# Performance work log

Measured on AMD Instinct MI355X. Metric: run time of the kernel, lower is better.

## Reference

```python
import jax, jax.numpy as jnp
import numpy as np

B, S, D, H = 2, 2048, 768, 12
DK = D // H


def setup_inputs() -> dict:
    key = jax.random.key(0)
    ks = jax.random.split(key, 11)
    sc = 1.0 / np.sqrt(D)
    return {
        "q": jax.random.normal(ks[0], (B, S, D), jnp.float32),
        "k": jax.random.normal(ks[1], (B, S, D), jnp.float32),
        "v": jax.random.normal(ks[2], (B, S, D), jnp.float32),
        "Wq": jax.random.normal(ks[3], (D, D), jnp.float32) * sc,
        "bq": jnp.zeros((D,), jnp.float32),
        "Wk": jax.random.normal(ks[4], (D, D), jnp.float32) * sc,
        "bk": jnp.zeros((D,), jnp.float32),
        "Wv": jax.random.normal(ks[5], (D, D), jnp.float32) * sc,
        "bv": jnp.zeros((D,), jnp.float32),
        "Wc": jax.random.normal(ks[6], (D, D), jnp.float32) * sc,
        "bc": jnp.zeros((D,), jnp.float32),
    }


def _split(t):
    # Faithful to source: view(B, n_head, S, d_k) WITHOUT transpose —
    # heads partition the flattened (S*D) buffer, not the feature axis.
    return t.reshape(B, H, S, DK)


def reference(q, k, v, Wq, bq, Wk, bk, Wv, bv, Wc, bc):
    q = _split(q @ Wq.T + bq)  # [B,H,S,DK]
    k = _split(k @ Wk.T + bk)
    v = _split(v @ Wv.T + bv)
    score = jnp.einsum("bhqd,bhkd->bhqk", q, k) / np.sqrt(DK)  # [B,H,S,S]
    attn = jax.nn.softmax(score, axis=-1)
    # Faithful bug in source: uses pre-softmax score, not attn.
    out = jnp.einsum("bhqk,bhkd->bhqd", score, v)  # [B,H,S,DK]
    out = out.transpose(0, 2, 1, 3).reshape(B, S, D)  # concat
    out = out @ Wc.T + bc
    return out, attn
```

## Files before the change

kernel.cpp:

```cpp
#include <hip/hip_runtime.h>
#include <hip/hip_bf16.h>


#define S_LEN   2048
#define D_MODEL 768
#define NHEAD   12
#define DKH     64
#define BSROWS  4096
#define HEADSZ  (S_LEN * DKH)
#define WELEMS  (D_MODEL * D_MODEL)

typedef __attribute__((ext_vector_type(4))) float f32x4;
typedef __attribute__((ext_vector_type(8))) short s16x8;

static __device__ __forceinline__ unsigned cvtpk(float lo, float hi) {
    unsigned r;
    asm("v_cvt_pk_bf16_f32 %0, %1, %2" : "=v"(r) : "v"(lo), "v"(hi));
    return r;
}

static __device__ __forceinline__ short f2bf(float f) {
    return (short)cvtpk(f, f);
}

static __device__ __forceinline__ s16x8 cvt8(f32x4 a, f32x4 b) {
    union { unsigned u[4]; s16x8 v; } o;
    o.u[0] = cvtpk(a[0], a[1]);
    o.u[1] = cvtpk(a[2], a[3]);
    o.u[2] = cvtpk(b[0], b[1]);
    o.u[3] = cvtpk(b[2], b[3]);
    return o.v;
}

static __device__ __forceinline__ void gload16(const void* g, void* l) {
    __builtin_amdgcn_global_load_lds((const __attribute__((address_space(1))) void*)g,
                                     (__attribute__((address_space(3))) void*)l, 16, 0, 0);
}

static __device__ __forceinline__ s16x8 ldfrag(const short* tile, int row, int c16) {
    int byte = row * 128 + ((c16 * 16) ^ ((row & 7) << 4));
    return *(const s16x8*)((const char*)tile + byte);
}

__global__ __launch_bounds__(256) void prep_w(const float* __restrict__ W0,
                                              const float* __restrict__ W1,
                                              const float* __restrict__ W2,
                                              const float* __restrict__ W3,
                                              short* __restrict__ dst)
{
    const float* src = (blockIdx.y == 0) ? W0 : (blockIdx.y == 1) ? W1
                     : (blockIdx.y == 2) ? W2 : W3;
    short* d = dst + (size_t)blockIdx.y * WELEMS;
    int i = (blockIdx.x * 256 + threadIdx.x) * 8;
    f32x4 a = *(const f32x4*)(src + i);
    f32x4 b = *(const f32x4*)(src + i + 4);
    *(s16x8*)(d + i) = cvt8(a, b);
}

template<int A_F32, int OUT_F32>
static __device__ __forceinline__ void gemm_body128(const void* __restrict__ Av,
                                                    const short* __restrict__ Wb,
                                                    const float* __restrict__ bias,
                                                    void* __restrict__ Cv,
                                                    int mt, int nt)
{
    __shared__ short As[8192];
    __shared__ short Bs[8192];
    const int t = threadIdx.x, w = t >> 6, lane = t & 63;
    const int lrow = lane & 15, lgrp = lane >> 4;
    const int wr = w >> 1, wc = w & 1;

    f32x4 acc[4][4];
#pragma unroll
    for (int m = 0; m < 4; ++m)
#pragma unroll
        for (int n = 0; n < 4; ++n) acc[m][n] = {0.f, 0.f, 0.f, 0.f};

    for (int kk = 0; kk < 768; kk += 64) {
        __syncthreads();
#pragma unroll
        for (int j = 0; j < 4; ++j) {
            int cid = t + j * 256, row = cid >> 3, ch = cid & 7;
            gload16(Wb + (size_t)(nt * 128 + row) * 768 + kk + ((ch ^ (row & 7)) * 8),
                    (char*)Bs + j * 4096 + w * 1024);
        }
        if (A_F32) {
#pragma unroll
            for (int j = 0; j < 2; ++j) {
                int cid = t + j * 256, row = cid >> 2, q4 = cid & 3;
                const float* src = (const float*)Av + (size_t)(mt * 128 + row) * 768 + kk + q4 * 16;
                f32x4 v0 = *(const f32x4*)(src);
                f32x4 v1 = *(const f32x4*)(src + 4);
                f32x4 v2 = *(const f32x4*)(src + 8);
                f32x4 v3 = *(const f32x4*)(src + 12);
                int c0 = q4 * 2;
                *(s16x8*)((char*)As + row * 128 + (((c0    ) ^ (row & 7)) * 16)) = cvt8(v0, v1);
                *(s16x8*)((char*)As + row * 128 + (((c0 + 1) ^ (row & 7)) * 16)) = cvt8(v2, v3);
            }
        } else {
#pragma unroll
            for (int j = 0; j < 4; ++j) {
                int cid = t + j * 256, row = cid >> 3, ch = cid & 7;
                gload16((const short*)Av + (size_t)(mt * 128 + row) * 768 + kk + ((ch ^ (row & 7)) * 8),
                        (char*)As + j * 4096 + w * 1024);
            }
        }
        __syncthreads();
#pragma unroll
        for (int kc = 0; kc < 2; ++kc) {
            s16x8 af[4], bfr[4];
#pragma unroll
            for (int m = 0; m < 4; ++m) af[m] = ldfrag(As, wr * 64 + m * 16 + lrow, kc * 4 + lgrp);
#pragma unroll
            for (int n = 0; n < 4; ++n) bfr[n] = ldfrag(Bs, wc * 64 + n * 16 + lrow, kc * 4 + lgrp);
            __builtin_amdgcn_s_setprio(1);
#pragma unroll
            for (int m = 0; m < 4; ++m)
#pragma unroll
                for (int n = 0; n < 4; ++n)
                    acc[m][n] = __builtin_amdgcn_mfma_f32_16x16x32_bf16(af[m], bfr[n], acc[m][n], 0, 0, 0);
            __builtin_amdgcn_s_setprio(0);
        }
    }
#pragma unroll
    for (int n = 0; n < 4; ++n) {
        int col = nt * 128 + wc * 64 + n * 16 + lrow;
        float bvv = bias[col];
#pragma unroll
        for (int m = 0; m < 4; ++m)
#pragma unroll
            for (int r = 0; r < 4; ++r) {
                int row = mt * 128 + wr * 64 + m * 16 + lgrp * 4 + r;
                float v = acc[m][n][r] + bvv;
                if (OUT_F32) ((float*)Cv)[(size_t)row * 768 + col] = v;
                else         ((short*)Cv)[(size_t)row * 768 + col] = f2bf(v);
            }
    }
}

template<int OUT_F32>
static __device__ __forceinline__ void gemm_body64(const short* __restrict__ Av,
                                                   const short* __restrict__ Wb,
                                                   const float* __restrict__ bias,
                                                   void* __restrict__ Cv,
                                                   int mt, int nt)
{
    __shared__ short As[4096];
    __shared__ short Bs[4096];
    const int t = threadIdx.x, w = t >> 6, lane = t & 63;
    const int lrow = lane & 15, lgrp = lane >> 4;
    const int wr = w >> 1, wc = w & 1;

    f32x4 acc[2][2];
#pragma unroll
    for (int m = 0; m < 2; ++m)
#pragma unroll
        for (int n = 0; n < 2; ++n) acc[m][n] = {0.f, 0.f, 0.f, 0.f};

    for (int kk = 0; kk < 768; kk += 64) {
        __syncthreads();
#pragma unroll
        for (int j = 0; j < 2; ++j) {
            int cid = t + j * 256, row = cid >> 3, ch = cid & 7;
            int cs = (ch ^ (row & 7)) * 8;
            gload16(Av + (size_t)(mt * 64 + row) * 768 + kk + cs,
                    As + w * 512 + j * 2048);
            gload16(Wb + (size_t)(nt * 64 + row) * 768 + kk + cs,
                    Bs + w * 512 + j * 2048);
        }
        __syncthreads();
#pragma unroll
        for (int kc = 0; kc < 2; ++kc) {
            s16x8 af[2], bfr[2];
#pragma unroll
            for (int m = 0; m < 2; ++m) af[m] = ldfrag(As, wr * 32 + m * 16 + lrow, kc * 4 + lgrp);
#pragma unroll
            for (int n = 0; n < 2; ++n) bfr[n] = ldfrag(Bs, wc * 32 + n * 16 + lrow, kc * 4 + lgrp);
            __builtin_amdgcn_s_setprio(1);
#pragma unroll
            for (int m = 0; m < 2; ++m)
#pragma unroll
                for (int n = 0; n < 2; ++n)
                    acc[m][n] = __builtin_amdgcn_mfma_f32_16x16x32_bf16(af[m], bfr[n], acc[m][n], 0, 0, 0);
            __builtin_amdgcn_s_setprio(0);
        }
    }
#pragma unroll
    for (int n = 0; n < 2; ++n) {
        int col = nt * 64 + wc * 32 + n * 16 + lrow;
        float bvv = bias[col];
#pragma unroll
        for (int m = 0; m < 2; ++m)
#pragma unroll
            for (int r = 0; r < 4; ++r) {
                int row = mt * 64 + wr * 32 + m * 16 + lgrp * 4 + r;
                float v = acc[m][n][r] + bvv;
                if (OUT_F32) ((float*)Cv)[(size_t)row * 768 + col] = v;
                else         ((short*)Cv)[(size_t)row * 768 + col] = f2bf(v);
            }
    }
}

__global__ __launch_bounds__(256) void gemm_qkv(const float* __restrict__ q,
                                                const float* __restrict__ k,
                                                const float* __restrict__ v,
                                                const short* __restrict__ Wbf,
                                                const float* __restrict__ bq,
                                                const float* __restrict__ bk,
                                                const float* __restrict__ bv,
                                                short* __restrict__ Qw,
                                                short* __restrict__ Kw,
                                                short* __restrict__ Vw)
{
    const int bid = blockIdx.x;
    const int idx = bid >> 3;
    const int panel = (bid & 7) * 12 + idx / 6;
    const int nt = idx % 6;
    const int z = panel / 32, mt = panel % 32;
    const float* A; const float* bias; short* C;
    if (z == 0)      { A = q; bias = bq; C = Qw; }
    else if (z == 1) { A = k; bias = bk; C = Kw; }
    else             { A = v; bias = bv; C = Vw; }
    gemm_body128<1, 0>(A, Wbf + (size_t)z * WELEMS, bias, C, mt, nt);
}

__global__ __launch_bounds__(256) void gemm_out(const short* __restrict__ Ob,
                                                const short* __restrict__ Wcb,
                                                const float* __restrict__ bc,
                                                float* __restrict__ out)
{
    const int bid = blockIdx.x;
    const int idx = (bid & 7) * 96 + (bid >> 3);
    const int mt = idx / 12, nt = idx % 12;
    gemm_body64<1>(Ob, Wcb, bc, out, mt, nt);
}

__global__ __launch_bounds__(256) void vtrans(const short* __restrict__ Vw,
                                              short* __restrict__ Vt)
{
    const int sblk = blockIdx.x, bh = blockIdx.y;
    const short* src = Vw + (size_t)bh * HEADSZ;
    short* dst = Vt + (size_t)bh * HEADSZ;
    const int t = threadIdx.x;
#pragma unroll
    for (int j = 0; j < 2; ++j) {
        int cid = t + j * 256, dk = cid >> 3, ch = cid & 7;
        int s0 = sblk * 64 + ch * 8;
        s16x8 vv;
#pragma unroll
        for (int e = 0; e < 8; ++e) vv[e] = src[(size_t)(s0 + e) * DKH + dk];
        *(s16x8*)(dst + (size_t)dk * S_LEN + s0) = vv;
    }
}

__global__ __launch_bounds__(256, 4) void attn_fused2(const short* __restrict__ Qb,
                                                      const short* __restrict__ Kb,
                                                      const short* __restrict__ Vtb,
                                                      short* __restrict__ Ob,
                                                      float* __restrict__ attn)
{
    __shared__ short lds[20480];
    short* Qs = lds;
    const float CE = 0.18033688f;

    const int bid = blockIdx.x;
    const int swz = (bid & 7) * 96 + (bid >> 3);
    const int qb = swz & 31, bh = swz >> 5;
    const int t = threadIdx.x, w = t >> 6, lane = t & 63;
    const int lrow = lane & 15, lgrp = lane >> 4;
    const int qh = w & 1, kh = w >> 1;
    const int b = bh / NHEAD, h = bh % NHEAD;
    const short* Qh = Qb + (size_t)bh * HEADSZ;
    const short* Kh = Kb + (size_t)bh * HEADSZ;
    const short* Vth = Vtb + (size_t)bh * HEADSZ;
    const int q0 = qb * 64;

#define STAGE_K4(dst, kt) do {                                                  \
    _Pragma("unroll")                                                           \
    for (int j = 0; j < 2; ++j) {                                               \
        int cid = t + j * 256, row = cid >> 3, ch = cid & 7;                    \
        gload16(Kh + (size_t)((kt) * 64 + row) * DKH + ((ch ^ (row & 7)) * 8),  \
                (dst) + w * 512 + j * 2048);                                    \
    } } while (0)

#define STAGE_V4(dst, kt) do {                                                  \
    _Pragma("unroll")                                                           \
    for (int j = 0; j < 2; ++j) {                                               \
        int cid = t + j * 256, row = cid >> 3, ch = cid & 7;                    \
        gload16(Vth + (size_t)row * S_LEN + (kt) * 64 + ((ch ^ (row & 7)) * 8), \
                (dst) + w * 512 + j * 2048);                                    \
    } } while (0)

#pragma unroll
    for (int j = 0; j < 2; ++j) {
        int cid = t + j * 256, row = cid >> 3, ch = cid & 7;
        gload16(Qh + (size_t)(q0 + row) * DKH + ((ch ^ (row & 7)) * 8),
                Qs + w * 512 + j * 2048);
    }
    STAGE_K4(lds + 4096, 0);
    STAGE_V4(lds + 12288, 0);
    __syncthreads();

    s16x8 aqA[2][2], aqB[2];
#pragma unroll
    for (int m = 0; m < 2; ++m)
#pragma unroll
        for (int c = 0; c < 2; ++c)
            aqA[m][c] = ldfrag(Qs, qh * 32 + m * 16 + lrow, c * 4 + lgrp);
#pragma unroll
    for (int c = 0; c < 2; ++c)
        aqB[c] = ldfrag(Qs, w * 16 + lrow, c * 4 + lgrp);
    __syncthreads();

    f32x4 pv[2][4];
#pragma unroll
    for (int m = 0; m < 2; ++m)
#pragma unroll
        for (int n = 0; n < 4; ++n) pv[m][n] = {0.f, 0.f, 0.f, 0.f};
    float zp[2] = {0.f, 0.f};

    short* SW = lds + w * 1024;
    int cur = 0;

    for (int kt = 0; kt < 32; ++kt) {
        if (kt) __syncthreads();
        if (kt < 31) {
            STAGE_K4(lds + 4096 + (cur ^ 1) * 4096, kt + 1);
            STAGE_V4(lds + 12288 + (cur ^ 1) * 4096, kt + 1);
        }
        const short* Kc = lds + 4096 + cur * 4096;
        const short* Vc = lds + 12288 + cur * 4096;

        f32x4 s[2][2];
#pragma unroll
        for (int m = 0; m < 2; ++m)
#pragma unroll
            for (int n = 0; n < 2; ++n) s[m][n] = {0.f, 0.f, 0.f, 0.f};
        __builtin_amdgcn_s_setprio(1);
#pragma unroll
        for (int n = 0; n < 2; ++n)
#pragma unroll
            for (int c = 0; c < 2; ++c) {
                s16x8 bk = ldfrag(Kc, kh * 32 + n * 16 + lrow, c * 4 + lgrp);
                s[0][n] = __builtin_amdgcn_mfma_f32_16x16x32_bf16(bk, aqA[0][c], s[0][n], 0, 0, 0);
                s[1][n] = __builtin_amdgcn_mfma_f32_16x16x32_bf16(bk, aqA[1][c], s[1][n], 0, 0, 0);
            }
        __builtin_amdgcn_s_setprio(0);

#pragma unroll
        for (int m = 0; m < 2; ++m) {
            int qlocal = m * 16 + lrow;
            int X = ((lrow >> 2) & 3) << 4;
#pragma unroll
            for (int n = 0; n < 2; ++n) {
#pragma unroll
                for (int r = 0; r < 4; ++r)
                    zp[m] += exp2f(s[m][n][r] * CE);
                unsigned lo = cvtpk(s[m][n][0] * 0.125f, s[m][n][1] * 0.125f);
                unsigned hi = cvtpk(s[m][n][2] * 0.125f, s[m][n][3] * 0.125f);
                *(unsigned long long*)((char*)SW + qlocal * 64 +
                                       ((n * 32 + lgrp * 8) ^ X))
                    = ((unsigned long long)hi << 32) | lo;
            }
        }

        s16x8 asb[2];
#pragma unroll
        for (int m = 0; m < 2; ++m) {
            int row = m * 16 + lrow;
            asb[m] = *(const s16x8*)((char*)SW + row * 64 +
                                     ((lgrp * 16) ^ ((((row >> 2) & 3)) << 4)));
        }
        __builtin_amdgcn_s_setprio(1);
#pragma unroll
        for (int n = 0; n < 4; ++n) {
            s16x8 bv = ldfrag(Vc, n * 16 + lrow, kh * 4 + lgrp);
            pv[0][n] = __builtin_amdgcn_mfma_f32_16x16x32_bf16(asb[0], bv, pv[0][n], 0, 0, 0);
            pv[1][n] = __builtin_amdgcn_mfma_f32_16x16x32_bf16(asb[1], bv, pv[1][n], 0, 0, 0);
        }
        __builtin_amdgcn_s_setprio(0);
        cur ^= 1;
    }
    __syncthreads();

    float* fvz = (float*)lds;
    float* pvx = (float*)(lds + 12288);
#pragma unroll
    for (int m = 0; m < 2; ++m) {
        float z = zp[m];
        z += __shfl_xor(z, 16, 64);
        z += __shfl_xor(z, 32, 64);
        if (lane < 16)
            fvz[kh * 64 + qh * 32 + m * 16 + lrow] = z;
    }
    if (kh == 1) {
        float* dst = pvx + qh * 2048 + lane * 4;
#pragma unroll
        for (int m = 0; m < 2; ++m)
#pragma unroll
            for (int n = 0; n < 4; ++n)
                *(f32x4*)(dst + (m * 4 + n) * 256) = pv[m][n];
    }
    __syncthreads();

    STAGE_K4(lds + 4096, 0);
    STAGE_K4(lds + 8192, 1);

    if (kh == 0) {
        const float* src = pvx + qh * 2048 + lane * 4;
#pragma unroll
        for (int m = 0; m < 2; ++m)
#pragma unroll
            for (int n = 0; n < 4; ++n) {
                pv[m][n] += *(const f32x4*)(src + (m * 4 + n) * 256);
#pragma unroll
                for (int r = 0; r < 4; ++r) {
                    int srow = q0 + qh * 32 + m * 16 + lgrp * 4 + r;
                    Ob[((size_t)b * S_LEN + srow) * D_MODEL + h * DKH + n * 16 + lrow]
                        = f2bf(pv[m][n][r]);
                }
            }
    }

    float ztot = fvz[w * 16 + lrow] + fvz[64 + w * 16 + lrow];
    float l2invz = -__log2f(ztot);

    float* aw = attn + (size_t)bh * S_LEN * S_LEN;
    for (int kt2 = 0; kt2 < 32; kt2 += 2) {
        __syncthreads();
        if (kt2 + 2 < 32) {
            STAGE_K4(lds + 4096 + ((kt2 + 2) & 3) * 4096, kt2 + 2);
            STAGE_K4(lds + 4096 + ((kt2 + 3) & 3) * 4096, kt2 + 3);
        }
#pragma unroll
        for (int u = 0; u < 2; ++u) {
            const int kt = kt2 + u;
            const short* Kc = lds + 4096 + (kt & 3) * 4096;
#pragma unroll
            for (int n = 0; n < 4; ++n) {
                f32x4 s = {0.f, 0.f, 0.f, 0.f};
                __builtin_amdgcn_s_setprio(1);
#pragma unroll
                for (int c = 0; c < 2; ++c) {
                    s16x8 bk = ldfrag(Kc, n * 16 + lrow, c * 4 + lgrp);
                    s = __builtin_amdgcn_mfma_f32_16x16x32_bf16(bk, aqB[c], s, 0, 0, 0);
                }
                __builtin_amdgcn_s_setprio(0);
                f32x4 a0;
#pragma unroll
                for (int r = 0; r < 4; ++r)
                    a0[r] = exp2f(fmaf(s[r], CE, l2invz));
                int kbase = kt * 64 + n * 16 + lgrp * 4;
                *(f32x4*)(aw + (size_t)(q0 + w * 16 + lrow) * S_LEN + kbase) = a0;
            }
        }
    }
#undef STAGE_K4
#undef STAGE_V4
}

extern "C" void kernel_launch(void* const* d_in, const int* in_sizes, int n_in,
                              void* d_out, int out_size, void* d_ws, size_t ws_size,
                              hipStream_t stream)
{
    const float* q  = (const float*)d_in[0];
    const float* k  = (const float*)d_in[1];
    const float* v  = (const float*)d_in[2];
    const float* Wq = (const float*)d_in[3];
    const float* bq = (const float*)d_in[4];
    const float* Wk = (const float*)d_in[5];
    const float* bk = (const float*)d_in[6];
    const float* Wv = (const float*)d_in[7];
    const float* bv = (const float*)d_in[8];
    const float* Wc = (const float*)d_in[9];
    const float* bc = (const float*)d_in[10];

    float* out  = (float*)d_out;
    float* attn = out + (size_t)BSROWS * D_MODEL;

    short* Wbf  = (short*)d_ws;
    short* Qw   = Wbf + (size_t)4 * WELEMS;
    short* Kw   = Qw + (size_t)BSROWS * D_MODEL;
    short* VwOb = Kw + (size_t)BSROWS * D_MODEL;
    short* Vt   = VwOb + (size_t)BSROWS * D_MODEL;

    prep_w<<<dim3(288, 4), dim3(256), 0, stream>>>(Wq, Wk, Wv, Wc, Wbf);

    gemm_qkv<<<dim3(576), dim3(256), 0, stream>>>(q, k, v, Wbf, bq, bk, bv,
                                                  Qw, Kw, VwOb);

    vtrans<<<dim3(32, 24), dim3(256), 0, stream>>>(VwOb, Vt);

    attn_fused2<<<dim3(768), dim3(256), 0, stream>>>(Qw, Kw, Vt, VwOb , attn);

    gemm_out<<<dim3(768), dim3(256), 0, stream>>>(VwOb , Wbf + (size_t)3 * WELEMS,
                                                  bc, out);
}
```

Before: 200.6 us.

## Retile QKV GEMM to 128x96 and load V fragments directly from global

The QKV projection GEMM moves from 128x128 to 128x96 tiles, giving 768 blocks instead of 576 for better CU balance, and its templates are specialised. In the attention kernel, V tiles are no longer staged through LDS. Each wave reads its V fragments straight from global memory into registers, which removes the LDS traffic for V. The attention launch-bounds occupancy hint drops from 4 to 3 blocks. The direct global V loads are not prefetched, so their latency may be exposed inside the loop.

```diff
diff --git a/kernel.cpp b/kernel.cpp
--- a/kernel.cpp
+++ b/kernel.cpp
@@ -57,146 +57,71 @@
     *(s16x8*)(d + i) = cvt8(a, b);
 }
 
-template<int A_F32, int OUT_F32>
-static __device__ __forceinline__ void gemm_body128(const void* __restrict__ Av,
-                                                    const short* __restrict__ Wb,
-                                                    const float* __restrict__ bias,
-                                                    void* __restrict__ Cv,
-                                                    int mt, int nt)
+static __device__ __forceinline__ void gemm_qkv_body(const float* __restrict__ Av,
+                                                     const short* __restrict__ Wb,
+                                                     const float* __restrict__ bias,
+                                                     short* __restrict__ Cv,
+                                                     int mt, int nt)
 {
     __shared__ short As[8192];
-    __shared__ short Bs[8192];
+    __shared__ short Bs[6144];
     const int t = threadIdx.x, w = t >> 6, lane = t & 63;
     const int lrow = lane & 15, lgrp = lane >> 4;
     const int wr = w >> 1, wc = w & 1;
 
-    f32x4 acc[4][4];
+    f32x4 acc[4][3];
 #pragma unroll
     for (int m = 0; m < 4; ++m)
 #pragma unroll
-        for (int n = 0; n < 4; ++n) acc[m][n] = {0.f, 0.f, 0.f, 0.f};
+        for (int n = 0; n < 3; ++n) acc[m][n] = {0.f, 0.f, 0.f, 0.f};
 
     for (int kk = 0; kk < 768; kk += 64) {
         __syncthreads();
 #pragma unroll
-        for (int j = 0; j < 4; ++j) {
+        for (int j = 0; j < 3; ++j) {
             int cid = t + j * 256, row = cid >> 3, ch = cid & 7;
-            gload16(Wb + (size_t)(nt * 128 + row) * 768 + kk + ((ch ^ (row & 7)) * 8),
+            gload16(Wb + (size_t)(nt * 96 + row) * 768 + kk + ((ch ^ (row & 7)) * 8),
                     (char*)Bs + j * 4096 + w * 1024);
         }
-        if (A_F32) {
-#pragma unroll
-            for (int j = 0; j < 2; ++j) {
-                int cid = t + j * 256, row = cid >> 2, q4 = cid & 3;
-                const float* src = (const float*)Av + (size_t)(mt * 128 + row) * 768 + kk + q4 * 16;
-                f32x4 v0 = *(const f32x4*)(src);
-                f32x4 v1 = *(const f32x4*)(src + 4);
-                f32x4 v2 = *(const f32x4*)(src + 8);
-                f32x4 v3 = *(const f32x4*)(src + 12);
-                int c0 = q4 * 2;
-                *(s16x8*)((char*)As + row * 128 + (((c0    ) ^ (row & 7)) * 16)) = cvt8(v0, v1);
-                *(s16x8*)((char*)As + row * 128 + (((c0 + 1) ^ (row & 7)) * 16)) = cvt8(v2, v3);
-            }
-        } else {
-#pragma unroll
-            for (int j = 0; j < 4; ++j) {
-                int cid = t + j * 256, row = cid >> 3, ch = cid & 7;
-                gload16((const short*)Av + (size_t)(mt * 128 + row) * 768 + kk + ((ch ^ (row & 7)) * 8),
-                        (char*)As + j * 4096 + w * 1024);
-            }
+#pragma unroll
+        for (int j = 0; j < 2; ++j) {
+            int cid = t + j * 256, row = cid >> 2, q4 = cid & 3;
+            const float* src = Av + (size_t)(mt * 128 + row) * 768 + kk + q4 * 16;
+            f32x4 v0 = *(const f32x4*)(src);
+            f32x4 v1 = *(const f32x4*)(src + 4);
+            f32x4 v2 = *(const f32x4*)(src + 8);
+            f32x4 v3 = *(const f32x4*)(src + 12);
+            int c0 = q4 * 2;
+            *(s16x8*)((char*)As + row * 128 + (((c0    ) ^ (row & 7)) * 16)) = cvt8(v0, v1);
+            *(s16x8*)((char*)As + row * 128 + (((c0 + 1) ^ (row & 7)) * 16)) = cvt8(v2, v3);
         }
         __syncthreads();
 #pragma unroll
         for (int kc = 0; kc < 2; ++kc) {
-            s16x8 af[4], bfr[4];
+            s16x8 af[4], bfr[3];
 #pragma unroll
             for (int m = 0; m < 4; ++m) af[m] = ldfrag(As, wr * 64 + m * 16 + lrow, kc * 4 + lgrp);
 #pragma unroll
-            for (int n = 0; n < 4; ++n) bfr[n] = ldfrag(Bs, wc * 64 + n * 16 + lrow, kc * 4 + lgrp);
+            for (int n = 0; n < 3; ++n) bfr[n] = ldfrag(Bs, wc * 48 + n * 16 + lrow, kc * 4 + lgrp);
             __builtin_amdgcn_s_setprio(1);
 #pragma unroll
             for (int m = 0; m < 4; ++m)
 #pragma unroll
-                for (int n = 0; n < 4; ++n)
+                for (int n = 0; n < 3; ++n)
                     acc[m][n] = __builtin_amdgcn_mfma_f32_16x16x32_bf16(af[m], bfr[n], acc[m][n], 0, 0, 0);
             __builtin_amdgcn_s_setprio(0);
         }
     }
 #pragma unroll
-    for (int n = 0; n < 4; ++n) {
-        int col = nt * 128 + wc * 64 + n * 16 + lrow;
+    for (int n = 0; n < 3; ++n) {
+        int col = nt * 96 + wc * 48 + n * 16 + lrow;
         float bvv = bias[col];
 #pragma unroll
         for (int m = 0; m < 4; ++m)
 #pragma unroll
             for (int r = 0; r < 4; ++r) {
                 int row = mt * 128 + wr * 64 + m * 16 + lgrp * 4 + r;
-                float v = acc[m][n][r] + bvv;
-                if (OUT_F32) ((float*)Cv)[(size_t)row * 768 + col] = v;
-                else         ((short*)Cv)[(size_t)row * 768 + col] = f2bf(v);
-            }
-    }
-}
-
-template<int OUT_F32>
-static __device__ __forceinline__ void gemm_body64(const short* __restrict__ Av,
-                                                   const short* __restrict__ Wb,
-                                                   const float* __restrict__ bias,
-                                                   void* __restrict__ Cv,
-                                                   int mt, int nt)
-{
-    __shared__ short As[4096];
-    __shared__ short Bs[4096];
-    const int t = threadIdx.x, w = t >> 6, lane = t & 63;
-    const int lrow = lane & 15, lgrp = lane >> 4;
-    const int wr = w >> 1, wc = w & 1;
-
-    f32x4 acc[2][2];
-#pragma unroll
-    for (int m = 0; m < 2; ++m)
-#pragma unroll
-        for (int n = 0; n < 2; ++n) acc[m][n] = {0.f, 0.f, 0.f, 0.f};
-
-    for (int kk = 0; kk < 768; kk += 64) {
-        __syncthreads();
-#pragma unroll
-        for (int j = 0; j < 2; ++j) {
-            int cid = t + j * 256, row = cid >> 3, ch = cid & 7;
-            int cs = (ch ^ (row & 7)) * 8;
-            gload16(Av + (size_t)(mt * 64 + row) * 768 + kk + cs,
-                    As + w * 512 + j * 2048);
-            gload16(Wb + (size_t)(nt * 64 + row) * 768 + kk + cs,
-                    Bs + w * 512 + j * 2048);
-        }
-        __syncthreads();
-#pragma unroll
-        for (int kc = 0; kc < 2; ++kc) {
-            s16x8 af[2], bfr[2];
-#pragma unroll
-            for (int m = 0; m < 2; ++m) af[m] = ldfrag(As, wr * 32 + m * 16 + lrow, kc * 4 + lgrp);
-#pragma unroll
-            for (int n = 0; n < 2; ++n) bfr[n] = ldfrag(Bs, wc * 32 + n * 16 + lrow, kc * 4 + lgrp);
-            __builtin_amdgcn_s_setprio(1);
-#pragma unroll
-            for (int m = 0; m < 2; ++m)
-#pragma unroll
-                for (int n = 0; n < 2; ++n)
-                    acc[m][n] = __builtin_amdgcn_mfma_f32_16x16x32_bf16(af[m], bfr[n], acc[m][n], 0, 0, 0);
-            __builtin_amdgcn_s_setprio(0);
-        }
-    }
-#pragma unroll
-    for (int n = 0; n < 2; ++n) {
-        int col = nt * 64 + wc * 32 + n * 16 + lrow;
-        float bvv = bias[col];
-#pragma unroll
-        for (int m = 0; m < 2; ++m)
-#pragma unroll
-            for (int r = 0; r < 4; ++r) {
-                int row = mt * 64 + wr * 32 + m * 16 + lgrp * 4 + r;
-                float v = acc[m][n][r] + bvv;
-                if (OUT_F32) ((float*)Cv)[(size_t)row * 768 + col] = v;
-                else         ((short*)Cv)[(size_t)row * 768 + col] = f2bf(v);
+                Cv[(size_t)row * 768 + col] = f2bf(acc[m][n][r] + bvv);
             }
     }
 }
@@ -214,14 +139,74 @@
 {
     const int bid = blockIdx.x;
     const int idx = bid >> 3;
-    const int panel = (bid & 7) * 12 + idx / 6;
-    const int nt = idx % 6;
+    const int panel = (bid & 7) * 12 + idx / 8;
+    const int nt = idx & 7;
     const int z = panel / 32, mt = panel % 32;
     const float* A; const float* bias; short* C;
     if (z == 0)      { A = q; bias = bq; C = Qw; }
     else if (z == 1) { A = k; bias = bk; C = Kw; }
     else             { A = v; bias = bv; C = Vw; }
-    gemm_body128<1, 0>(A, Wbf + (size_t)z * WELEMS, bias, C, mt, nt);
+    gemm_qkv_body(A, Wbf + (size_t)z * WELEMS, bias, C, mt, nt);
+}
+
+static __device__ __forceinline__ void gemm_body64(const short* __restrict__ Av,
+                                                   const short* __restrict__ Wb,
+                                                   const float* __restrict__ bias,
+                                                   float* __restrict__ Cv,
+                                                   int mt, int nt)
+{
+    __shared__ short As[4096];
+    __shared__ short Bs[4096];
+    const int t = threadIdx.x, w = t >> 6, lane = t & 63;
+    const int lrow = lane & 15, lgrp = lane >> 4;
+    const int wr = w >> 1, wc = w & 1;
+
+    f32x4 acc[2][2];
+#pragma unroll
+    for (int m = 0; m < 2; ++m)
+#pragma unroll
+        for (int n = 0; n < 2; ++n) acc[m][n] = {0.f, 0.f, 0.f, 0.f};
+
+    for (int kk = 0; kk < 768; kk += 64) {
+        __syncthreads();
+#pragma unroll
+        for (int j = 0; j < 2; ++j) {
+            int cid = t + j * 256, row = cid >> 3, ch = cid & 7;
+            int cs = (ch ^ (row & 7)) * 8;
+            gload16(Av + (size_t)(mt * 64 + row) * 768 + kk + cs,
+                    As + w * 512 + j * 2048);
+            gload16(Wb + (size_t)(nt * 64 + row) * 768 + kk + cs,
+                    Bs + w * 512 + j * 2048);
+        }
+        __syncthreads();
+#pragma unroll
+        for (int kc = 0; kc < 2; ++kc) {
+            s16x8 af[2], bfr[2];
+#pragma unroll
+            for (int m = 0; m < 2; ++m) af[m] = ldfrag(As, wr * 32 + m * 16 + lrow, kc * 4 + lgrp);
+#pragma unroll
+            for (int n = 0; n < 2; ++n) bfr[n] = ldfrag(Bs, wc * 32 + n * 16 + lrow, kc * 4 + lgrp);
+            __builtin_amdgcn_s_setprio(1);
+#pragma unroll
+            for (int m = 0; m < 2; ++m)
+#pragma unroll
+                for (int n = 0; n < 2; ++n)
+                    acc[m][n] = __builtin_amdgcn_mfma_f32_16x16x32_bf16(af[m], bfr[n], acc[m][n], 0, 0, 0);
+            __builtin_amdgcn_s_setprio(0);
+        }
+    }
+#pragma unroll
+    for (int n = 0; n < 2; ++n) {
+        int col = nt * 64 + wc * 32 + n * 16 + lrow;
+        float bvv = bias[col];
+#pragma unroll
+        for (int m = 0; m < 2; ++m)
+#pragma unroll
+            for (int r = 0; r < 4; ++r) {
+                int row = mt * 64 + wr * 32 + m * 16 + lgrp * 4 + r;
+                Cv[(size_t)row * 768 + col] = acc[m][n][r] + bvv;
+            }
+    }
 }
 
 __global__ __launch_bounds__(256) void gemm_out(const short* __restrict__ Ob,
@@ -232,7 +217,7 @@
     const int bid = blockIdx.x;
     const int idx = (bid & 7) * 96 + (bid >> 3);
     const int mt = idx / 12, nt = idx % 12;
-    gemm_body64<1>(Ob, Wcb, bc, out, mt, nt);
+    gemm_body64(Ob, Wcb, bc, out, mt, nt);
 }
 
 __global__ __launch_bounds__(256) void vtrans(const short* __restrict__ Vw,
@@ -253,7 +238,7 @@
     }
 }
 
-__global__ __launch_bounds__(256, 4) void attn_fused2(const short* __restrict__ Qb,
+__global__ __launch_bounds__(256, 3) void attn_fused2(const short* __restrict__ Qb,
                                                       const short* __restrict__ Kb,
                                                       const short* __restrict__ Vtb,
                                                       short* __restrict__ Ob,
@@ -283,14 +268,6 @@
                 (dst) + w * 512 + j * 2048);                                    \
     } } while (0)
 
-#define STAGE_V4(dst, kt) do {                                                  \
-    _Pragma("unroll")                                                           \
-    for (int j = 0; j < 2; ++j) {                                               \
-        int cid = t + j * 256, row = cid >> 3, ch = cid & 7;                    \
-        gload16(Vth + (size_t)row * S_LEN + (kt) * 64 + ((ch ^ (row & 7)) * 8), \
-                (dst) + w * 512 + j * 2048);                                    \
-    } } while (0)
-
 #pragma unroll
     for (int j = 0; j < 2; ++j) {
         int cid = t + j * 256, row = cid >> 3, ch = cid & 7;
@@ -298,7 +275,6 @@
                 Qs + w * 512 + j * 2048);
     }
     STAGE_K4(lds + 4096, 0);
-    STAGE_V4(lds + 12288, 0);
     __syncthreads();
 
     s16x8 aqA[2][2], aqB[2];
@@ -324,12 +300,15 @@
 
     for (int kt = 0; kt < 32; ++kt) {
         if (kt) __syncthreads();
-        if (kt < 31) {
-            STAGE_K4(lds + 4096 + (cur ^ 1) * 4096, kt + 1);
-            STAGE_V4(lds + 12288 + (cur ^ 1) * 4096, kt + 1);
-        }
+        if (kt < 31) STAGE_K4(lds + 4096 + (cur ^ 1) * 4096, kt + 1);
+
+        s16x8 vv[4];
+#pragma unroll
+        for (int n = 0; n < 4; ++n)
+            vv[n] = *(const s16x8*)(Vth + (size_t)(n * 16 + lrow) * S_LEN
+                                    + kt * 64 + (kh * 4 + lgrp) * 8);
+
         const short* Kc = lds + 4096 + cur * 4096;
-        const short* Vc = lds + 12288 + cur * 4096;
 
         f32x4 s[2][2];
 #pragma unroll
@@ -374,9 +353,8 @@
         __builtin_amdgcn_s_setprio(1);
 #pragma unroll
         for (int n = 0; n < 4; ++n) {
-            s16x8 bv = ldfrag(Vc, n * 16 + lrow, kh * 4 + lgrp);
-            pv[0][n] = __builtin_amdgcn_mfma_f32_16x16x32_bf16(asb[0], bv, pv[0][n], 0, 0, 0);
-            pv[1][n] = __builtin_amdgcn_mfma_f32_16x16x32_bf16(asb[1], bv, pv[1][n], 0, 0, 0);
+            pv[0][n] = __builtin_amdgcn_mfma_f32_16x16x32_bf16(asb[0], vv[n], pv[0][n], 0, 0, 0);
+            pv[1][n] = __builtin_amdgcn_mfma_f32_16x16x32_bf16(asb[1], vv[n], pv[1][n], 0, 0, 0);
         }
         __builtin_amdgcn_s_setprio(0);
         cur ^= 1;
@@ -456,7 +434,6 @@
         }
     }
 #undef STAGE_K4
-#undef STAGE_V4
 }
 
 extern "C" void kernel_launch(void* const* d_in, const int* in_sizes, int n_in,
@@ -486,7 +463,7 @@
 
     prep_w<<<dim3(288, 4), dim3(256), 0, stream>>>(Wq, Wk, Wv, Wc, Wbf);
 
-    gemm_qkv<<<dim3(576), dim3(256), 0, stream>>>(q, k, v, Wbf, bq, bk, bv,
+    gemm_qkv<<<dim3(768), dim3(256), 0, stream>>>(q, k, v, Wbf, bq, bk, bv,
                                                   Qw, Kw, VwOb);
 
     vtrans<<<dim3(32, 24), dim3(256), 0, stream>>>(VwOb, Vt);
```

Result: slower. 211.7 us (+5.5%).
